# Kernel tuning notes

Hardware: AMD Instinct MI355X
Metric: run time of the kernel (lower is better)

Reference implementation:

```python
import jax, jax.numpy as jnp
import numpy as np

L = 4          # num transformer layers
C = 128        # embed_dim
P = 16         # patch size
NH = 8         # num heads
HD = C // NH   # head dim
SCALE = HD ** -0.5
THRESH = [0.001, 0.0012, 0.0015, 0.002]
EPS = 1e-5


def _ln(x, w, b):
    mu = jnp.mean(x, -1, keepdims=True)
    v = jnp.mean(jnp.square(x - mu), -1, keepdims=True)
    return (x - mu) * jax.lax.rsqrt(v + EPS) * w + b


def _attn(x, qw, qb, ow, ob):
    B, N, _ = x.shape
    qkv = (x @ qw + qb).reshape(B, N, 3, NH, HD)
    q, k, v = jnp.moveaxis(qkv, 2, 0)                      # each [B,N,NH,HD]
    q = q.transpose(0, 2, 1, 3)
    k = k.transpose(0, 2, 1, 3)
    v = v.transpose(0, 2, 1, 3)                            # [B,NH,N,HD]
    probs = jax.nn.softmax(jnp.einsum('bhnd,bhmd->bhnm', q, k) * SCALE, axis=-1)
    o = jnp.einsum('bhnm,bhmd->bhnd', probs, v).transpose(0, 2, 1, 3).reshape(B, N, C)
    return o @ ow + ob, probs


def _layer(x, i, ln1_w, ln1_b, qkv_w, qkv_b, out_w, out_b, ln2_w, ln2_b, w1, b1, w2, b2):
    a, probs = _attn(_ln(x, ln1_w[i], ln1_b[i]), qkv_w[i], qkv_b[i], out_w[i], out_b[i])
    x = x + a
    h = jax.nn.gelu(_ln(x, ln2_w[i], ln2_b[i]) @ w1[i] + b1[i], approximate=False)
    return x + h @ w2[i] + b2[i], probs


def forward(conv_w, conv_b, cls_token, pos_embed, ln1_w, ln1_b, qkv_w, qkv_b,
            out_w, out_b, ln2_w, ln2_b, mlp_w1, mlp_b1, mlp_w2, mlp_b2, x, meta=None):
    B = x.shape[0]
    Hh, Ww = x.shape[2] // P, x.shape[3] // P
    # patch embed == conv with kernel=stride=P, expressed as a patch matmul
    xr = x.reshape(B, 3, Hh, P, Ww, P).transpose(0, 2, 4, 1, 3, 5).reshape(B, Hh * Ww, 3 * P * P)
    tok = xr @ conv_w.reshape(C, -1).T + conv_b           # [B, nH*nW, C]
    x = jnp.concatenate([jnp.broadcast_to(cls_token, (B, 1, C)), tok], axis=1) + pos_embed
    meta_out = []
    for i in range(L):
        x, probs = _layer(x, i, ln1_w, ln1_b, qkv_w, qkv_b, out_w, out_b,
                          ln2_w, ln2_b, mlp_w1, mlp_b1, mlp_w2, mlp_b2)
        if i < L - 1:
            cls_t, tokens = x[:, :1], x[:, 1:]
            if meta is None:
                am = jnp.mean(probs[:, :, 1:, 0], axis=1)  # [B, N] attn of tokens to cls
                keep = am > THRESH[i]
                fb = keep.sum(1) == 0                      # fallback: keep argmax token
                keep = keep | (fb[:, None] & (jnp.arange(am.shape[1])[None, :] == jnp.argmax(am, 1)[:, None]))
                count = keep.sum(1)
                order = jnp.argsort(~keep, axis=1)         # stable: kept tokens first, in order
                mk = int(jnp.max(count))
                order, count = np.asarray(order), np.asarray(count)
                meta_out.append((order, count, mk))
            else:
                order, count, mk = meta[i]
            g = jnp.take_along_axis(tokens, jnp.asarray(order[:, :mk])[:, :, None], axis=1)
            valid = (jnp.arange(mk)[None, :] < jnp.asarray(count)[:, None]).astype(tokens.dtype)
            x = jnp.concatenate([cls_t, g * valid[:, :, None]], axis=1)
            # original re-adds pos_embed[0:1+mk] regardless of which tokens survived
            x = x + jnp.concatenate([pos_embed[:, :1], pos_embed[:, 1:1 + mk]], axis=1)
    return x, meta_out


def setup_inputs() -> dict:
    key = jax.random.key(0)
    ks = jax.random.split(key, 8)
    def w(k, shape, fan_in):
        return jax.random.normal(k, shape, jnp.float32) / np.float32(np.sqrt(fan_in))
    N_POS = (512 // P) * (512 // P) + 1  # 1025
    return {
        'conv_w': w(ks[0], (C, 3, P, P), 3 * P * P),
        'conv_b': jnp.zeros((C,), jnp.float32),
        'cls_token': jnp.zeros((1, 1, C), jnp.float32),
        'pos_embed': 0.02 * jax.random.truncated_normal(ks[1], -2.0, 2.0, (1, N_POS, C), jnp.float32),
        'ln1_w': jnp.ones((L, C), jnp.float32), 'ln1_b': jnp.zeros((L, C), jnp.float32),
        'qkv_w': w(ks[2], (L, C, 3 * C), C), 'qkv_b': jnp.zeros((L, 3 * C), jnp.float32),
        'out_w': w(ks[3], (L, C, C), C), 'out_b': jnp.zeros((L, C), jnp.float32),
        'ln2_w': jnp.ones((L, C), jnp.float32), 'ln2_b': jnp.zeros((L, C), jnp.float32),
        'mlp_w1': w(ks[4], (L, C, 4 * C), C), 'mlp_b1': jnp.zeros((L, 4 * C), jnp.float32),
        'mlp_w2': w(ks[5], (L, 4 * C, C), 4 * C), 'mlp_b2': jnp.zeros((L, C), jnp.float32),
        'x': jax.random.normal(ks[6], (8, 3, 512, 512), jnp.float32),
    }


def reference(conv_w, conv_b, cls_token, pos_embed, ln1_w, ln1_b, qkv_w, qkv_b,
              out_w, out_b, ln2_w, ln2_b, mlp_w1, mlp_b1, mlp_w2, mlp_b2, x):
    out, _ = forward(conv_w, conv_b, cls_token, pos_embed, ln1_w, ln1_b, qkv_w, qkv_b,
                     out_w, out_b, ln2_w, ln2_b, mlp_w1, mlp_b1, mlp_w2, mlp_b2, x)
    return out
```

## Files before the change

### kernel.cpp

```cpp
#include <hip/hip_runtime.h>
#include <hip/hip_bf16.h>
#include <math.h>

typedef __hip_bfloat16 bf16;
typedef __attribute__((ext_vector_type(4))) _Float16 half4;
typedef __attribute__((ext_vector_type(4))) float f32x4;

#define NMAX 1025
#define TMAX 1024
#define BATCH 8
#define CH 128
#define NHEAD 8
#define HDIM 16
#define MMAX (BATCH * NMAX)
#define QGRID 17
#define VSTRIDE 1028
#define POSZ 1049600
#define KCHUNK 192

__device__ __forceinline__ float b2f(bf16 v) { return __bfloat162float(v); }

__device__ __forceinline__ bool is_bf16(const void* ln1w_raw) {
    return ((const unsigned*)ln1w_raw)[0] == 0x3F803F80u;
}
__device__ __forceinline__ float ldsel(const void* p, size_t i, bool bf) {
    return bf ? __bfloat162float(((const bf16*)p)[i]) : ((const float*)p)[i];
}

struct CvtDesc { const void* src; float* dst; int cnt; };
struct CvtPack { CvtDesc d[15]; };

__global__ void convert_kernel(CvtPack p, const void* ln1w_raw, int* nTok) {
    bool bf = is_bf16(ln1w_raw);
    CvtDesc dd = p.d[blockIdx.y];
    int idx = blockIdx.x * 256 + threadIdx.x;
    if (idx < dd.cnt) dd.dst[idx] = ldsel(dd.src, idx, bf);
    if (blockIdx.y == 0 && idx == 0) nTok[0] = NMAX;
}

__global__ void prep_kernel(const void* conv_w, float* __restrict__ wT,
                            const void* ln1w_raw) {
    bool bf = is_bf16(ln1w_raw);
    int idx = blockIdx.x * 256 + threadIdx.x;
    if (idx < 768 * 128) {
        int k = idx >> 7, oc = idx & 127;
        wT[idx] = ldsel(conv_w, (size_t)oc * 768 + k, bf);
    }
}

__global__ __launch_bounds__(256) void patch_partial(
        const void* __restrict__ img, const float* __restrict__ wT,
        float* __restrict__ partial, const void* ln1w_raw) {
    __shared__ float pbuf[8 * KCHUNK];
    bool bf = is_bf16(ln1w_raw);
    int b = blockIdx.y;
    int g = blockIdx.x & 127;
    int kc = blockIdx.x >> 7;
    int tid = threadIdx.x;
    int t0 = g * 8;
    int kbase = kc * KCHUNK;
    const int NV = 8 * KCHUNK / 4;
    for (int i = tid; i < NV; i += 256) {
        int e = i << 2;
        int t = e / KCHUNK, kloc = e - t * KCHUNK;
        int k = kbase + kloc;
        int c = k >> 8, rem = k & 255, p1 = rem >> 4, p2 = rem & 15;
        int hw = t0 + t;
        int h = hw >> 5, w = hw & 31;
        size_t a = (((size_t)(b * 3 + c) * 512) + h * 16 + p1) * 512 + w * 16 + p2;
        float4 v;
        if (bf) {
            ushort4 u = *(const ushort4*)((const unsigned short*)img + a);
            v.x = __uint_as_float((unsigned)u.x << 16);
            v.y = __uint_as_float((unsigned)u.y << 16);
            v.z = __uint_as_float((unsigned)u.z << 16);
            v.w = __uint_as_float((unsigned)u.w << 16);
        } else {
            v = *(const float4*)((const float*)img + a);
        }
        *(float4*)&pbuf[e] = v;
    }
    __syncthreads();
    int team = tid >> 7;
    int col = tid & 127;
    float acc[4];
#pragma unroll
    for (int t = 0; t < 4; t++) acc[t] = 0.f;
    const float* wc = wT + (size_t)kbase * 128;
    const float* pb = pbuf + team * 4 * KCHUNK;
    for (int k4 = 0; k4 < KCHUNK; k4 += 4) {
        float w0 = wc[(k4 + 0) * 128 + col];
        float w1 = wc[(k4 + 1) * 128 + col];
        float w2 = wc[(k4 + 2) * 128 + col];
        float w3 = wc[(k4 + 3) * 128 + col];
#pragma unroll
        for (int t = 0; t < 4; t++) {
            const float4 a = *(const float4*)&pb[t * KCHUNK + k4];
            acc[t] = fmaf(a.x, w0, acc[t]);
            acc[t] = fmaf(a.y, w1, acc[t]);
            acc[t] = fmaf(a.z, w2, acc[t]);
            acc[t] = fmaf(a.w, w3, acc[t]);
        }
    }
    float* pp = partial + ((size_t)(kc * 8 + b) * 1024 + t0 + team * 4) * 128 + col;
#pragma unroll
    for (int t = 0; t < 4; t++) pp[(size_t)t * 128] = acc[t];
}

__global__ __launch_bounds__(256) void patch_reduce(
        const float* __restrict__ partial, const float* __restrict__ conv_b,
        const float* __restrict__ cls_tok, const float* __restrict__ pos,
        float* __restrict__ out) {
    if (blockIdx.x == 4096) {
        for (int i = threadIdx.x; i < 8 * 128; i += 256) {
            int b = i >> 7, c = i & 127;
            out[(size_t)(b * NMAX) * CH + c] = cls_tok[c] + pos[c];
        }
        return;
    }
    int idx = blockIdx.x * 256 + threadIdx.x;
    int tg = idx >> 7;
    int col = idx & 127;
    int b = tg >> 10, tok = tg & 1023;
    size_t pi = ((size_t)b * 1024 + tok) * 128 + col;
    const size_t PSTRIDE = (size_t)8 * 1024 * 128;
    float v = partial[pi] + partial[pi + PSTRIDE]
            + partial[pi + 2 * PSTRIDE] + partial[pi + 3 * PSTRIDE];
    out[((size_t)(b * NMAX) + 1 + tok) * CH + col] =
        v + conv_b[col] + pos[(size_t)(1 + tok) * CH + col];
}

template <int K, int NCOL, int CTILE, int ROWS, int TEAMS, bool LN,
          bool GELU_ACT, bool RESID, bool QKV_SPLIT>
__global__ void mm_kernel(const float* __restrict__ A, const float* __restrict__ W,
                          const float* __restrict__ bias, const float* __restrict__ lnw,
                          const float* __restrict__ lnb, const float* __restrict__ R,
                          float* __restrict__ out, _Float16* __restrict__ kout,
                          _Float16* __restrict__ vout, const int* __restrict__ nPtr) {
    __shared__ float As[ROWS * K];
    const int THREADS = CTILE * TEAMS;
    const int RPT = ROWS / TEAMS;
    int N = nPtr[0];
    int M = BATCH * N;
    int row0 = blockIdx.x * ROWS;
    if (row0 >= M) return;
    int tid = threadIdx.x;
    for (int i = tid; i < ROWS * K / 4; i += THREADS) {
        int e = i << 2;
        int r = e / K, rem = e % K;
        float4 v;
        int row = row0 + r;
        if (row < M)
            v = *(const float4*)&A[(size_t)row * K + rem];
        else
            v = make_float4(0.f, 0.f, 0.f, 0.f);
        *(float4*)&As[r * K + rem] = v;
    }
    __syncthreads();
    if (LN) {
        int wid = tid >> 6, lane = tid & 63;
        const int NW = THREADS / 64;
        float wl0 = lnw[lane], wl1 = lnw[64 + lane];
        float bl0 = lnb[lane], bl1 = lnb[64 + lane];
        for (int r = wid; r < ROWS; r += NW) {
            float x0 = As[r * K + lane], x1 = As[r * K + 64 + lane];
            float s = x0 + x1;
#pragma unroll
            for (int off = 32; off; off >>= 1) s += __shfl_xor(s, off);
            float mu = s * (1.f / 128.f);
            float d0 = x0 - mu, d1 = x1 - mu;
            float v = d0 * d0 + d1 * d1;
#pragma unroll
            for (int off = 32; off; off >>= 1) v += __shfl_xor(v, off);
            float inv = 1.f / sqrtf(v * (1.f / 128.f) + 1e-5f);
            As[r * K + lane] = d0 * inv * wl0 + bl0;
            As[r * K + 64 + lane] = d1 * inv * wl1 + bl1;
        }
        __syncthreads();
    }
    int team = tid / CTILE;
    int col = tid % CTILE;
    const float* At = As + team * RPT * K;
    float acc[RPT];
#pragma unroll
    for (int r = 0; r < RPT; r++) acc[r] = 0.f;
    for (int k4 = 0; k4 < K; k4 += 4) {
        float w0 = W[(size_t)(k4 + 0) * NCOL + col];
        float w1 = W[(size_t)(k4 + 1) * NCOL + col];
        float w2 = W[(size_t)(k4 + 2) * NCOL + col];
        float w3 = W[(size_t)(k4 + 3) * NCOL + col];
#pragma unroll
        for (int r = 0; r < RPT; r++) {
            const float4 a = *(const float4*)&At[r * K + k4];
            acc[r] = fmaf(a.x, w0, acc[r]);
            acc[r] = fmaf(a.y, w1, acc[r]);
            acc[r] = fmaf(a.z, w2, acc[r]);
            acc[r] = fmaf(a.w, w3, acc[r]);
        }
    }
    float bv = bias[col];
    int rbase = row0 + team * RPT;
    int rmax = min(RPT, M - rbase);
    if (QKV_SPLIT) {
        int part = col >> 7;
        int c128 = col & 127;
        int hh = c128 >> 4, dd = c128 & 15;
        for (int r = 0; r < rmax; r++) {
            float v = acc[r] + bv;
            int row = rbase + r;
            if (part == 0) {
                out[(size_t)row * 128 + c128] = v;
            } else {
                int bb = row / N, nn = row - (row / N) * N;
                if (part == 1) {
                    _Float16 hi = (_Float16)v;
                    _Float16 lo = (_Float16)(v - (float)hi);
                    size_t kb2 = ((size_t)(bb * 8 + hh) * NMAX + nn) * 32 + dd;
                    kout[kb2] = hi;
                    kout[kb2 + 16] = lo;
                } else {
                    vout[((size_t)(bb * 8 + hh) * 16 + dd) * VSTRIDE + nn] = (_Float16)v;
                }
            }
        }
        if (blockIdx.x == 0 && part == 2) {
            int zn = min(16, VSTRIDE - N);
            for (int bb = 0; bb < 8; bb++) {
                size_t rb = ((size_t)((bb * 8 + hh) * 16 + dd)) * VSTRIDE;
                for (int i = 0; i < zn; i++) vout[rb + N + i] = (_Float16)0.f;
            }
            if (hh == 7 && dd == 15) {
                for (int i = 0; i < 16; i++)
                    vout[(size_t)1024 * VSTRIDE + i] = (_Float16)0.f;
            }
        }
    } else {
        for (int r = 0; r < rmax; r++) {
            float v = acc[r] + bv;
            if (GELU_ACT) v = 0.5f * v * (1.f + erff(v * 0.70710678118654752f));
            if (RESID) v += R[(size_t)(rbase + r) * NCOL + col];
            out[(size_t)(rbase + r) * NCOL + col] = v;
        }
    }
}

__global__ __launch_bounds__(256) void attn_kernel(
        const float* __restrict__ qbuf, const _Float16* __restrict__ kbuf,
        const _Float16* __restrict__ vbuf, float* __restrict__ oout,
        float* __restrict__ clsp, const int* __restrict__ nPtr) {
    int N = nPtr[0];
    int bid = blockIdx.x;
    int b = bid & 7;
    int h = (bid >> 3) & 7;
    int qg = bid >> 6;
    int wave = threadIdx.x >> 6;
    int lane = threadIdx.x & 63;
    int qt = qg * 4 + wave;
    if (qt * 16 >= N) return;
    int ql = lane & 15;
    int hig = lane >> 4;
    int nq = qt * 16 + ql;
    int nqc = min(nq, N - 1);
    half4 qhi, qlo;
    {
        const float4 qv = *(const float4*)(qbuf + ((size_t)(b * N + nqc)) * 128 + h * HDIM + hig * 4);
        float q0 = qv.x * 0.25f, q1 = qv.y * 0.25f, q2 = qv.z * 0.25f, q3 = qv.w * 0.25f;
        qhi[0] = (_Float16)q0; qlo[0] = (_Float16)(q0 - (float)qhi[0]);
        qhi[1] = (_Float16)q1; qlo[1] = (_Float16)(q1 - (float)qhi[1]);
        qhi[2] = (_Float16)q2; qlo[2] = (_Float16)(q2 - (float)qhi[2]);
        qhi[3] = (_Float16)q3; qlo[3] = (_Float16)(q3 - (float)qhi[3]);
    }
    const _Float16* kb = kbuf + (size_t)(b * 8 + h) * NMAX * 32;
    const _Float16* vt = vbuf + ((size_t)(b * 8 + h) * 16 + ql) * VSTRIDE;
    f32x4 of = {0.f, 0.f, 0.f, 0.f};
    const f32x4 zz = {0.f, 0.f, 0.f, 0.f};
    float m = -3.0e38f, l = 0.f, s0raw = 0.f;
    int ntFull = N >> 4;
    int t = 0;
    for (; t + 2 <= ntFull; t += 2) {
        int k0 = t * 16;
        const _Float16* kpA = kb + ((size_t)(k0 + ql)) * 32 + hig * 4;
        const _Float16* kpB = kpA + 16 * 32;
        half4 khiA = *(const half4*)(kpA);
        half4 kloA = *(const half4*)(kpA + 16);
        half4 khiB = *(const half4*)(kpB);
        half4 kloB = *(const half4*)(kpB + 16);
        f32x4 sA1 = __builtin_amdgcn_mfma_f32_16x16x16f16(khiA, qhi, zz, 0, 0, 0);
        f32x4 sB1 = __builtin_amdgcn_mfma_f32_16x16x16f16(khiB, qhi, zz, 0, 0, 0);
        f32x4 sA2 = __builtin_amdgcn_mfma_f32_16x16x16f16(khiA, qlo, zz, 0, 0, 0);
        f32x4 sB2 = __builtin_amdgcn_mfma_f32_16x16x16f16(khiB, qlo, zz, 0, 0, 0);
        sA2 = __builtin_amdgcn_mfma_f32_16x16x16f16(kloA, qhi, sA2, 0, 0, 0);
        sB2 = __builtin_amdgcn_mfma_f32_16x16x16f16(kloB, qhi, sB2, 0, 0, 0);
        f32x4 saA = sA1 + sA2;
        f32x4 saB = sB1 + sB2;
        if (t == 0) s0raw = saA[0];
        float mcA = fmaxf(fmaxf(saA[0], saA[1]), fmaxf(saA[2], saA[3]));
        float mcB = fmaxf(fmaxf(saB[0], saB[1]), fmaxf(saB[2], saB[3]));
        float mloc = fmaxf(mcA, mcB);
        if (!__all(mloc <= m + 8.f)) {
            float mc = fmaxf(mloc, __shfl_xor(mloc, 16));
            mc = fmaxf(mc, __shfl_xor(mc, 32));
            float mnew = fmaxf(m, mc);
            float corr = __expf(m - mnew);
            l *= corr;
#pragma unroll
            for (int r = 0; r < 4; r++)
                of[r] *= __shfl(corr, hig * 4 + r);
            m = mnew;
        }
        float pA0 = __expf(saA[0] - m), pA1 = __expf(saA[1] - m);
        float pA2 = __expf(saA[2] - m), pA3 = __expf(saA[3] - m);
        float pB0 = __expf(saB[0] - m), pB1 = __expf(saB[1] - m);
        float pB2 = __expf(saB[2] - m), pB3 = __expf(saB[3] - m);
        l += ((pA0 + pA1) + (pA2 + pA3)) + ((pB0 + pB1) + (pB2 + pB3));
        half4 pfA, pfB;
        pfA[0] = (_Float16)pA0; pfA[1] = (_Float16)pA1;
        pfA[2] = (_Float16)pA2; pfA[3] = (_Float16)pA3;
        pfB[0] = (_Float16)pB0; pfB[1] = (_Float16)pB1;
        pfB[2] = (_Float16)pB2; pfB[3] = (_Float16)pB3;
        half4 vfA = *(const half4*)(vt + k0 + hig * 4);
        half4 vfB = *(const half4*)(vt + k0 + 16 + hig * 4);
        of = __builtin_amdgcn_mfma_f32_16x16x16f16(pfA, vfA, of, 0, 0, 0);
        of = __builtin_amdgcn_mfma_f32_16x16x16f16(pfB, vfB, of, 0, 0, 0);
    }
    if (t < ntFull) {
        int k0 = t * 16;
        const _Float16* kp = kb + ((size_t)(k0 + ql)) * 32 + hig * 4;
        half4 khi = *(const half4*)(kp);
        half4 klo = *(const half4*)(kp + 16);
        f32x4 s1 = __builtin_amdgcn_mfma_f32_16x16x16f16(khi, qhi, zz, 0, 0, 0);
        f32x4 s2 = __builtin_amdgcn_mfma_f32_16x16x16f16(khi, qlo, zz, 0, 0, 0);
        s2 = __builtin_amdgcn_mfma_f32_16x16x16f16(klo, qhi, s2, 0, 0, 0);
        f32x4 sa = s1 + s2;
        if (t == 0) s0raw = sa[0];
        float mloc = fmaxf(fmaxf(sa[0], sa[1]), fmaxf(sa[2], sa[3]));
        if (!__all(mloc <= m + 8.f)) {
            float mc = fmaxf(mloc, __shfl_xor(mloc, 16));
            mc = fmaxf(mc, __shfl_xor(mc, 32));
            float mnew = fmaxf(m, mc);
            float corr = __expf(m - mnew);
            l *= corr;
#pragma unroll
            for (int r = 0; r < 4; r++)
                of[r] *= __shfl(corr, hig * 4 + r);
            m = mnew;
        }
        float p0 = __expf(sa[0] - m), p1 = __expf(sa[1] - m);
        float p2 = __expf(sa[2] - m), p3 = __expf(sa[3] - m);
        l += (p0 + p1) + (p2 + p3);
        half4 pf;
        pf[0] = (_Float16)p0; pf[1] = (_Float16)p1;
        pf[2] = (_Float16)p2; pf[3] = (_Float16)p3;
        half4 vf = *(const half4*)(vt + k0 + hig * 4);
        of = __builtin_amdgcn_mfma_f32_16x16x16f16(pf, vf, of, 0, 0, 0);
        t++;
    }
    int k0t = ntFull * 16;
    if (k0t < N) {
        int kk = min(k0t + ql, N - 1);
        const _Float16* kp = kb + (size_t)kk * 32 + hig * 4;
        half4 khi = *(const half4*)(kp);
        half4 klo = *(const half4*)(kp + 16);
        f32x4 s1 = __builtin_amdgcn_mfma_f32_16x16x16f16(khi, qhi, zz, 0, 0, 0);
        f32x4 s2 = __builtin_amdgcn_mfma_f32_16x16x16f16(khi, qlo, zz, 0, 0, 0);
        s2 = __builtin_amdgcn_mfma_f32_16x16x16f16(klo, qhi, s2, 0, 0, 0);
        f32x4 sa = s1 + s2;
        if (ntFull == 0) s0raw = sa[0];
        float s0 = (k0t + hig * 4 + 0 < N) ? sa[0] : -3.0e38f;
        float s1m = (k0t + hig * 4 + 1 < N) ? sa[1] : -3.0e38f;
        float s2m = (k0t + hig * 4 + 2 < N) ? sa[2] : -3.0e38f;
        float s3m = (k0t + hig * 4 + 3 < N) ? sa[3] : -3.0e38f;
        float mloc = fmaxf(fmaxf(s0, s1m), fmaxf(s2m, s3m));
        if (!__all(mloc <= m + 8.f)) {
            float mc = fmaxf(mloc, __shfl_xor(mloc, 16));
            mc = fmaxf(mc, __shfl_xor(mc, 32));
            float mnew = fmaxf(m, mc);
            float corr = __expf(m - mnew);
            l *= corr;
#pragma unroll
            for (int r = 0; r < 4; r++)
                of[r] *= __shfl(corr, hig * 4 + r);
            m = mnew;
        }
        float p0 = __expf(s0 - m);
        float p1 = __expf(s1m - m);
        float p2 = __expf(s2m - m);
        float p3 = __expf(s3m - m);
        l += (p0 + p1) + (p2 + p3);
        half4 pf;
        pf[0] = (_Float16)p0; pf[1] = (_Float16)p1;
        pf[2] = (_Float16)p2; pf[3] = (_Float16)p3;
        half4 vf = *(const half4*)(vt + k0t + hig * 4);
        of = __builtin_amdgcn_mfma_f32_16x16x16f16(pf, vf, of, 0, 0, 0);
    }
    l += __shfl_xor(l, 16);
    l += __shfl_xor(l, 32);
    float linv = 1.f / l;
#pragma unroll
    for (int r = 0; r < 4; r++) {
        int qq = qt * 16 + hig * 4 + r;
        if (qq < N) {
            float ov = of[r] * __shfl(linv, hig * 4 + r);
            oout[((size_t)(b * N + qq)) * 128 + h * HDIM + ql] = ov;
        }
    }
    if (hig == 0 && nq >= 1 && nq < N) {
        clsp[(size_t)(b * 8 + h) * TMAX + (nq - 1)] = __expf(s0raw - m) * linv;
    }
}

__global__ __launch_bounds__(1024) void prune_kernel(const float* __restrict__ clsp,
                                                     int* __restrict__ order,
                                                     int* __restrict__ cnt,
                                                     const int* __restrict__ nPtr, int layer) {
    __shared__ int sdata[1024];
    __shared__ float wv_[16];
    __shared__ int wi_[16];
    __shared__ int wc_[16];
    __shared__ int sArg, sCnt0;
    int b = blockIdx.x;
    int t = threadIdx.x;
    int N = nPtr[0];
    int T = N - 1;
    float am = -1.f;
    if (t < T) {
        float s = 0.f;
#pragma unroll
        for (int h = 0; h < 8; h++) s += clsp[((size_t)(b * 8 + h)) * TMAX + t];
        am = s * 0.125f;
    }
    const double TH[4] = {0.001, 0.0012, 0.0015, 0.002};
    int keep = (t < T) && ((double)am > TH[layer]);
    float bv = am;
    int bi = t;
    int kc = keep;
#pragma unroll
    for (int off = 32; off; off >>= 1) {
        float ov = __shfl_xor(bv, off);
        int oi = __shfl_xor(bi, off);
        if (ov > bv || (ov == bv && oi < bi)) { bv = ov; bi = oi; }
        kc += __shfl_xor(kc, off);
    }
    int wid = t >> 6, lane = t & 63;
    if (lane == 0) { wv_[wid] = bv; wi_[wid] = bi; wc_[wid] = kc; }
    __syncthreads();
    if (t == 0) {
        float Bv = wv_[0];
        int Bi = wi_[0], C = 0;
        for (int w = 0; w < 16; w++) {
            C += wc_[w];
            if (wv_[w] > Bv || (wv_[w] == Bv && wi_[w] < Bi)) { Bv = wv_[w]; Bi = wi_[w]; }
        }
        sArg = Bi;
        sCnt0 = C;
    }
    __syncthreads();
    if (sCnt0 == 0) keep = (t == sArg) && (t < T);
    sdata[t] = keep;
    __syncthreads();
    for (int off = 1; off < 1024; off <<= 1) {
        int v = sdata[t];
        int add = (t >= off) ? sdata[t - off] : 0;
        __syncthreads();
        sdata[t] = v + add;
        __syncthreads();
    }
    int incl = sdata[t];
    int total = sdata[1023];
    if (t < T) {
        if (keep)
            order[b * TMAX + (incl - 1)] = t;
        else
            order[b * TMAX + total + t - incl] = t;
    }
    if (t == 0) cnt[b] = total;
}

__global__ __launch_bounds__(256) void gather_kernel(
        const float* __restrict__ xin, float* __restrict__ xout,
        const int* __restrict__ order, const int* __restrict__ cnt,
        const float* __restrict__ pos, const int* __restrict__ nPtr,
        int* __restrict__ nNext) {
    int Nold = nPtr[0];
    int mk = cnt[0];
#pragma unroll
    for (int i = 1; i < 8; i++) mk = max(mk, cnt[i]);
    int Nnew = mk + 1;
    if (blockIdx.x == 0 && blockIdx.y == 0 && threadIdx.x == 0) nNext[0] = Nnew;
    int b = blockIdx.y;
    int j = blockIdx.x * 2 + (threadIdx.x >> 7);
    int c = threadIdx.x & 127;
    if (j >= Nnew) return;
    float v;
    if (j == 0)
        v = xin[((size_t)(b * Nold)) * CH + c];
    else {
        int src = order[b * TMAX + (j - 1)];
        v = (j - 1 < cnt[b]) ? xin[((size_t)(b * Nold + 1 + src)) * CH + c] : 0.f;
    }
    xout[((size_t)(b * Nnew + j)) * CH + c] = v + pos[(size_t)j * CH + c];
}

__global__ void outconv_kernel(const float* __restrict__ xin, void* __restrict__ out,
                               int total, const void* ln1w_raw) {
    bool bf = is_bf16(ln1w_raw);
    int i = blockIdx.x * 256 + threadIdx.x;
    if (i < total) {
        if (bf) ((bf16*)out)[i] = __float2bfloat16(xin[i]);
        else    ((float*)out)[i] = xin[i];
    }
}

extern "C" void kernel_launch(void* const* d_in, const int* in_sizes, int n_in,
                              void* d_out, int out_size, void* d_ws, size_t ws_size,
                              hipStream_t stream) {
    const void* conv_w = d_in[0];
    const void* conv_b = d_in[1];
    const void* cls_token = d_in[2];
    const void* pos_embed = d_in[3];
    const void* ln1_w = d_in[4];
    const void* ln1_b = d_in[5];
    const void* qkv_w = d_in[6];
    const void* qkv_b = d_in[7];
    const void* out_w = d_in[8];
    const void* out_b = d_in[9];
    const void* ln2_w = d_in[10];
    const void* ln2_b = d_in[11];
    const void* mlp_w1 = d_in[12];
    const void* mlp_b1 = d_in[13];
    const void* mlp_w2 = d_in[14];
    const void* mlp_b2 = d_in[15];
    const void* img = d_in[16];

    float* ws = (float*)d_ws;
    size_t off = 0;
    float* bufA = ws + off; off += POSZ;
    float* bufB = ws + off; off += POSZ;
    float* obuf = ws + off; off += POSZ;
    float* tmp  = ws + off; off += (size_t)BATCH * NMAX * 512;
    float* wT   = ws + off; off += 768 * 128;
    float* clsp = ws + off; off += (size_t)BATCH * NHEAD * TMAX;
    int* order  = (int*)(ws + off); off += BATCH * TMAX;
    int* cnt    = (int*)(ws + off); off += 16;
    int* nTok   = (int*)(ws + off); off += 16;
    float* wts  = ws + off;
    const size_t wts_total = 924544;

    float* qbuf = tmp;
    _Float16* kbuf = (_Float16*)(tmp + POSZ);
    _Float16* vbuf = (_Float16*)(tmp + 2 * POSZ);

    float* f_conv_b = wts + 0;
    float* f_cls    = wts + 128;
    float* f_pos    = wts + 256;
    float* f_ln1w   = wts + 131456;
    float* f_ln1b   = wts + 131968;
    float* f_qkvw   = wts + 132480;
    float* f_qkvb   = wts + 329088;
    float* f_outw   = wts + 330624;
    float* f_outb   = wts + 396160;
    float* f_ln2w   = wts + 396672;
    float* f_ln2b   = wts + 397184;
    float* f_w1     = wts + 397696;
    float* f_b1     = wts + 659840;
    float* f_w2     = wts + 661888;
    float* f_b2     = wts + 924032;

    CvtPack pk;
    pk.d[0]  = {conv_b,    f_conv_b, 128};
    pk.d[1]  = {cls_token, f_cls,    128};
    pk.d[2]  = {pos_embed, f_pos,    131200};
    pk.d[3]  = {ln1_w,     f_ln1w,   512};
    pk.d[4]  = {ln1_b,     f_ln1b,   512};
    pk.d[5]  = {qkv_w,     f_qkvw,   196608};
    pk.d[6]  = {qkv_b,     f_qkvb,   1536};
    pk.d[7]  = {out_w,     f_outw,   65536};
    pk.d[8]  = {out_b,     f_outb,   512};
    pk.d[9]  = {ln2_w,     f_ln2w,   512};
    pk.d[10] = {ln2_b,     f_ln2b,   512};
    pk.d[11] = {mlp_w1,    f_w1,     262144};
    pk.d[12] = {mlp_b1,    f_b1,     2048};
    pk.d[13] = {mlp_w2,    f_w2,     262144};
    pk.d[14] = {mlp_b2,    f_b2,     512};

    convert_kernel<<<dim3(1024, 15), 256, 0, stream>>>(pk, ln1_w, nTok);
    prep_kernel<<<(768 * 128 + 255) / 256, 256, 0, stream>>>(conv_w, wT, ln1_w);
    patch_partial<<<dim3(512, BATCH), 256, 0, stream>>>(img, wT, tmp, ln1_w);
    patch_reduce<<<4097, 256, 0, stream>>>(tmp, f_conv_b, f_cls, f_pos, bufA);

    float* xc = bufA;
    float* xalt = bufB;
    const int GR8 = (MMAX + 7) / 8;

    for (int i = 0; i < 4; i++) {
        const int* nP = nTok + i;
        mm_kernel<128, 384, 384, 8, 1, true, false, false, true>
            <<<GR8, 384, 0, stream>>>(
            xc, f_qkvw + (size_t)i * 128 * 384, f_qkvb + i * 384,
            f_ln1w + i * 128, f_ln1b + i * 128, nullptr, qbuf, kbuf, vbuf, nP);
        attn_kernel<<<QGRID * 64, 256, 0, stream>>>(
            qbuf, kbuf, vbuf, qbuf, clsp, nP);
        mm_kernel<128, 128, 128, 8, 2, false, false, true, false>
            <<<GR8, 256, 0, stream>>>(
            qbuf, f_outw + (size_t)i * 128 * 128, f_outb + i * 128,
            nullptr, nullptr, xc, xalt, nullptr, nullptr, nP);
        mm_kernel<128, 512, 512, 8, 1, true, true, false, false>
            <<<GR8, 512, 0, stream>>>(
            xalt, f_w1 + (size_t)i * 128 * 512, f_b1 + i * 512,
            f_ln2w + i * 128, f_ln2b + i * 128, nullptr, tmp, nullptr, nullptr, nP);
        mm_kernel<512, 128, 128, 8, 2, false, false, true, false>
            <<<GR8, 256, 0, stream>>>(
            tmp, f_w2 + (size_t)i * 512 * 128, f_b2 + i * 128,
            nullptr, nullptr, xalt, xc, nullptr, nullptr, nP);
        if (i < 3) {
            prune_kernel<<<BATCH, 1024, 0, stream>>>(clsp, order, cnt, nP, i);
            gather_kernel<<<dim3((NMAX + 1) / 2, BATCH), 256, 0, stream>>>(
                xc, xalt, order, cnt, f_pos, nP, nTok + i + 1);
            float* t2 = xc; xc = xalt; xalt = t2;
        }
    }
    outconv_kernel<<<(out_size + 255) / 256, 256, 0, stream>>>(xc, d_out, out_size, ln1_w);
}
```

Measured before the change: 576.1 us.

## Split attention key range across block waves and merge partial softmax in LDS

Each block now handles a single 16-query tile, and its four waves each process a quarter of the key tiles instead of four separate query tiles. The partial max, sum and output of each wave are written to shared memory and combined by wave 0 with the usual online-softmax rescaling. The grid grows to cover every query tile individually. The aim is to shorten each wave's serial loop over keys, which also helps when the token count shrinks after pruning. The cost is an extra block barrier, an LDS merge step and less reuse of K/V loads across waves.

```diff
diff --git a/kernel.cpp b/kernel.cpp
--- a/kernel.cpp
+++ b/kernel.cpp
@@ -13,7 +13,7 @@
 #define NHEAD 8
 #define HDIM 16
 #define MMAX (BATCH * NMAX)
-#define QGRID 17
+#define QTILES 65
 #define VSTRIDE 1028
 #define POSZ 1049600
 #define KCHUNK 192
@@ -248,15 +248,17 @@
         const float* __restrict__ qbuf, const _Float16* __restrict__ kbuf,
         const _Float16* __restrict__ vbuf, float* __restrict__ oout,
         float* __restrict__ clsp, const int* __restrict__ nPtr) {
+    __shared__ float sO[3][64][4];
+    __shared__ float sL[3][64];
+    __shared__ float sM[3][16];
     int N = nPtr[0];
     int bid = blockIdx.x;
     int b = bid & 7;
     int h = (bid >> 3) & 7;
-    int qg = bid >> 6;
+    int qt = bid >> 6;
+    if (qt * 16 >= N) return;
     int wave = threadIdx.x >> 6;
     int lane = threadIdx.x & 63;
-    int qt = qg * 4 + wave;
-    if (qt * 16 >= N) return;
     int ql = lane & 15;
     int hig = lane >> 4;
     int nq = qt * 16 + ql;
@@ -275,9 +277,14 @@
     f32x4 of = {0.f, 0.f, 0.f, 0.f};
     const f32x4 zz = {0.f, 0.f, 0.f, 0.f};
     float m = -3.0e38f, l = 0.f, s0raw = 0.f;
+    int ntAll = (N + 15) >> 4;
     int ntFull = N >> 4;
-    int t = 0;
-    for (; t + 2 <= ntFull; t += 2) {
+    int nqt = (ntAll + 3) >> 2;
+    int t0h = wave * nqt;
+    int t1h = min(ntAll, t0h + nqt);
+    int fullEnd = min(t1h, ntFull);
+    int t = t0h;
+    for (; t + 2 <= fullEnd; t += 2) {
         int k0 = t * 16;
         const _Float16* kpA = kb + ((size_t)(k0 + ql)) * 32 + hig * 4;
         const _Float16* kpB = kpA + 16 * 32;
@@ -323,7 +330,7 @@
         of = __builtin_amdgcn_mfma_f32_16x16x16f16(pfA, vfA, of, 0, 0, 0);
         of = __builtin_amdgcn_mfma_f32_16x16x16f16(pfB, vfB, of, 0, 0, 0);
     }
-    if (t < ntFull) {
+    if (t < fullEnd) {
         int k0 = t * 16;
         const _Float16* kp = kb + ((size_t)(k0 + ql)) * 32 + hig * 4;
         half4 khi = *(const half4*)(kp);
@@ -355,8 +362,8 @@
         of = __builtin_amdgcn_mfma_f32_16x16x16f16(pf, vf, of, 0, 0, 0);
         t++;
     }
-    int k0t = ntFull * 16;
-    if (k0t < N) {
+    if (t < t1h) {
+        int k0t = t * 16;
         int kk = min(k0t + ql, N - 1);
         const _Float16* kp = kb + (size_t)kk * 32 + hig * 4;
         half4 khi = *(const half4*)(kp);
@@ -365,7 +372,7 @@
         f32x4 s2 = __builtin_amdgcn_mfma_f32_16x16x16f16(khi, qlo, zz, 0, 0, 0);
         s2 = __builtin_amdgcn_mfma_f32_16x16x16f16(klo, qhi, s2, 0, 0, 0);
         f32x4 sa = s1 + s2;
-        if (ntFull == 0) s0raw = sa[0];
+        if (t == 0) s0raw = sa[0];
         float s0 = (k0t + hig * 4 + 0 < N) ? sa[0] : -3.0e38f;
         float s1m = (k0t + hig * 4 + 1 < N) ? sa[1] : -3.0e38f;
         float s2m = (k0t + hig * 4 + 2 < N) ? sa[2] : -3.0e38f;
@@ -395,17 +402,41 @@
     }
     l += __shfl_xor(l, 16);
     l += __shfl_xor(l, 32);
-    float linv = 1.f / l;
-#pragma unroll
-    for (int r = 0; r < 4; r++) {
-        int qq = qt * 16 + hig * 4 + r;
-        if (qq < N) {
-            float ov = of[r] * __shfl(linv, hig * 4 + r);
-            oout[((size_t)(b * N + qq)) * 128 + h * HDIM + ql] = ov;
-        }
-    }
-    if (hig == 0 && nq >= 1 && nq < N) {
-        clsp[(size_t)(b * 8 + h) * TMAX + (nq - 1)] = __expf(s0raw - m) * linv;
+    if (wave != 0) {
+        if (hig == 0) sM[wave - 1][ql] = m;
+        sL[wave - 1][lane] = l;
+        sO[wave - 1][lane][0] = of[0];
+        sO[wave - 1][lane][1] = of[1];
+        sO[wave - 1][lane][2] = of[2];
+        sO[wave - 1][lane][3] = of[3];
+    }
+    __syncthreads();
+    if (wave == 0) {
+        float m1 = sM[0][ql], m2 = sM[1][ql], m3 = sM[2][ql];
+        float M = fmaxf(fmaxf(m, m1), fmaxf(m2, m3));
+        float w0 = __expf(m - M), w1 = __expf(m1 - M);
+        float w2 = __expf(m2 - M), w3 = __expf(m3 - M);
+        float L = w0 * l + w1 * sL[0][lane] + w2 * sL[1][lane] + w3 * sL[2][lane];
+        float linv = 1.f / L;
+#pragma unroll
+        for (int r = 0; r < 4; r++) {
+            int qs = hig * 4 + r;
+            float W0 = __shfl(w0, qs);
+            float W1 = __shfl(w1, qs);
+            float W2 = __shfl(w2, qs);
+            float W3 = __shfl(w3, qs);
+            float Li = __shfl(linv, qs);
+            int qq = qt * 16 + qs;
+            if (qq < N) {
+                float ov = W0 * of[r] + W1 * sO[0][lane][r]
+                         + W2 * sO[1][lane][r] + W3 * sO[2][lane][r];
+                oout[((size_t)(b * N + qq)) * 128 + h * HDIM + ql] = ov * Li;
+            }
+        }
+        if (hig == 0 && nq >= 1 && nq < N) {
+            clsp[(size_t)(b * 8 + h) * TMAX + (nq - 1)] =
+                __expf(s0raw - m) * w0 * linv;
+        }
     }
 }
 
@@ -598,7 +629,7 @@
             <<<GR8, 384, 0, stream>>>(
             xc, f_qkvw + (size_t)i * 128 * 384, f_qkvb + i * 384,
             f_ln1w + i * 128, f_ln1b + i * 128, nullptr, qbuf, kbuf, vbuf, nP);
-        attn_kernel<<<QGRID * 64, 256, 0, stream>>>(
+        attn_kernel<<<QTILES * 64, 256, 0, stream>>>(
             qbuf, kbuf, vbuf, qbuf, clsp, nP);
         mm_kernel<128, 128, 128, 8, 2, false, false, true, false>
             <<<GR8, 256, 0, stream>>>(
```

After: 562.5 us. 2.4% less time.
